# Optimization experiments

Hardware: AMD Instinct MI355X
Metric: run time of the kernel (lower is better)

Reference implementation:

```python
import jax, jax.numpy as jnp
import numpy as np

B, A, M = 64, 128, 8          # batch (conformers), atoms, ensemble models
D, O0, O2, O4, O6 = 384, 256, 192, 160, 1  # AEV dim and padded layer out dims


def setup_inputs() -> dict:
    key = jax.random.key(0)
    ks = jax.random.split(key, 10)
    return {
        "species": jax.random.randint(ks[0], (B, A), 0, 4),
        "aev": jax.random.normal(ks[1], (B, A, D), dtype=jnp.float32),
        "w0": jax.random.normal(ks[2], (1, A, M, O0, D), dtype=jnp.float32),
        "b0": jax.random.normal(ks[3], (1, A, M, O0, 1), dtype=jnp.float32),
        "w2": jax.random.normal(ks[4], (1, A, M, O2, O0), dtype=jnp.float32),
        "b2": jax.random.normal(ks[5], (1, A, M, O2, 1), dtype=jnp.float32),
        "w4": jax.random.normal(ks[6], (1, A, M, O4, O2), dtype=jnp.float32),
        "b4": jax.random.normal(ks[7], (1, A, M, O4, 1), dtype=jnp.float32),
        "w6": jax.random.normal(ks[8], (1, A, M, O6, O4), dtype=jnp.float32),
        "b6": jax.random.normal(ks[9], (1, A, M, O6, 1), dtype=jnp.float32),
    }


def _celu(x, alpha=0.1):
    # F.celu(x, alpha) = max(0,x) + min(0, alpha*(exp(x/alpha)-1))
    return jnp.where(x > 0, x, alpha * jnp.expm1(x / alpha))


def reference(species, aev, w0, b0, w2, b2, w4, b4, w6, b6):
    # batchedLinear(v, W, b) == W @ v + b per (atom, model) block,
    # broadcast over batch; first layer broadcasts the model dim (1 -> M).
    # x: [B, A, M, out]
    x = jnp.einsum('zamoi,bai->bamo', w0, aev) + b0[..., 0]
    x = _celu(x)
    x = jnp.einsum('zamoi,bami->bamo', w2, x) + b2[..., 0]
    x = _celu(x)
    x = jnp.einsum('zamoi,bami->bamo', w4, x) + b4[..., 0]
    x = _celu(x)
    x = jnp.einsum('zamoi,bami->bamo', w6, x) + b6[..., 0]
    # sum over atoms, models, out (and the trailing singleton), divide by n_models
    energies = jnp.sum(x, axis=(1, 2, 3)) / M  # [B]
    return species, energies
```

## Files before the change

### kernel.cpp

```cpp
#include <hip/hip_runtime.h>

#define B_ 64
#define A_ 128
#define M_ 8
#define D_ 384
#define O0_ 256
#define O2_ 192
#define O4_ 160

typedef float f32x4 __attribute__((ext_vector_type(4)));
typedef _Float16 f16x8 __attribute__((ext_vector_type(8)));
typedef _Float16 f16x4 __attribute__((ext_vector_type(4)));

__device__ __forceinline__ float celu_f(float x) {
    return x > 0.f ? x : 0.1f * (__expf(x * 10.f) - 1.f);
}

__device__ __forceinline__ f32x4 zero4() {
    f32x4 v; v[0] = 0.f; v[1] = 0.f; v[2] = 0.f; v[3] = 0.f; return v;
}

template<int K, int O, int OPITCH, bool SWZ_OUT>
__device__ __forceinline__ void layer_mfma(const float* __restrict__ W,
                                           const float* __restrict__ bias,
                                           const _Float16* Xin, _Float16* Xout,
                                           int wave, int col, int quad)
{
    constexpr int KSTEPS = K / 32;
    constexpr int OTILES = O / 16;
    for (int ot = wave; ot < OTILES; ot += 4) {
        const float* wrow = W + (size_t)(ot * 16 + col) * K + quad * 8;
        f32x4 acc[4];
        #pragma unroll
        for (int nt = 0; nt < 4; ++nt) acc[nt] = zero4();
        #pragma unroll
        for (int ks = 0; ks < KSTEPS; ++ks) {
            f32x4 wlo = *(const f32x4*)(wrow + ks * 32);
            f32x4 whi = *(const f32x4*)(wrow + ks * 32 + 4);
            f16x8 afr;
            afr[0] = (_Float16)wlo[0]; afr[1] = (_Float16)wlo[1];
            afr[2] = (_Float16)wlo[2]; afr[3] = (_Float16)wlo[3];
            afr[4] = (_Float16)whi[0]; afr[5] = (_Float16)whi[1];
            afr[6] = (_Float16)whi[2]; afr[7] = (_Float16)whi[3];
            #pragma unroll
            for (int nt = 0; nt < 4; ++nt) {
                const int b = nt * 16 + col;
                const int c = ks * 4 + quad;
                const f16x8 bfr = *(const f16x8*)(Xin + b * K + ((c ^ (b & 7)) * 8));
                acc[nt] = __builtin_amdgcn_mfma_f32_16x16x32_f16(afr, bfr, acc[nt], 0, 0, 0);
            }
        }
        const f32x4 bias4 = *(const f32x4*)(bias + ot * 16 + quad * 4);
        const int o0 = ot * 16 + quad * 4;
        #pragma unroll
        for (int nt = 0; nt < 4; ++nt) {
            const int b = nt * 16 + col;
            f16x4 h;
            #pragma unroll
            for (int r = 0; r < 4; ++r) h[r] = (_Float16)celu_f(acc[nt][r] + bias4[r]);
            if (SWZ_OUT) {
                const int c = o0 >> 3;
                *(f16x4*)(Xout + b * OPITCH + ((c ^ (b & 7)) * 8) + (o0 & 7)) = h;
            } else {
                *(f16x4*)(Xout + b * OPITCH + o0) = h;
            }
        }
    }
}

__global__ __launch_bounds__(256, 2) void nn_kernel(
    const float* __restrict__ aev,
    const float* __restrict__ w0, const float* __restrict__ b0,
    const float* __restrict__ w2, const float* __restrict__ b2,
    const float* __restrict__ w4, const float* __restrict__ b4,
    const float* __restrict__ w6, const float* __restrict__ b6,
    float* __restrict__ out)
{
    __shared__ __align__(16) unsigned char smem_raw[57344];
    _Float16* const lds = (_Float16*)smem_raw;

    const int tid  = threadIdx.x;
    const int wave = tid >> 6;
    const int lane = tid & 63;
    const int col  = lane & 15;
    const int quad = lane >> 4;

    const int a  = blockIdx.x >> 3;
    const int m  = blockIdx.x & 7;
    const int am = a * 8 + m;

    const float* w0p = w0 + (size_t)am * O0_ * D_;
    const float* b0p = b0 + am * O0_;
    const float* w2p = w2 + (size_t)am * O2_ * O0_;
    const float* b2p = b2 + am * O2_;
    const float* w4p = w4 + (size_t)am * O4_ * O2_;
    const float* b4p = b4 + am * O4_;
    const float* w6p = w6 + am * O4_;
    const float  b6v = b6[am];

    _Float16* bufStage = lds;
    _Float16* X0 = lds + 12288;
    _Float16* X2 = lds;
    _Float16* X4 = lds + 12288;
    float* part = (float*)(smem_raw + 45568);

    f32x4 acc0[4][4];
    #pragma unroll
    for (int i = 0; i < 4; ++i)
        #pragma unroll
        for (int nt = 0; nt < 4; ++nt) acc0[i][nt] = zero4();

    #pragma unroll
    for (int kc = 0; kc < 2; ++kc) {
        if (kc) __syncthreads();
        #pragma unroll
        for (int it = 0; it < 6; ++it) {
            const int idx = tid + it * 256;
            const int b = idx / 24;
            const int c = idx % 24;
            const float* src = aev + ((size_t)b * A_ + a) * D_ + kc * 192 + c * 8;
            f32x4 lo = *(const f32x4*)src;
            f32x4 hi = *(const f32x4*)(src + 4);
            f16x8 h;
            h[0] = (_Float16)lo[0]; h[1] = (_Float16)lo[1];
            h[2] = (_Float16)lo[2]; h[3] = (_Float16)lo[3];
            h[4] = (_Float16)hi[0]; h[5] = (_Float16)hi[1];
            h[6] = (_Float16)hi[2]; h[7] = (_Float16)hi[3];
            *(f16x8*)(bufStage + b * 192 + ((c ^ (b & 7)) * 8)) = h;
        }
        __syncthreads();
        #pragma unroll
        for (int i = 0; i < 4; ++i) {
            const int ot = wave + i * 4;
            const float* wrow = w0p + (size_t)(ot * 16 + col) * D_ + kc * 192 + quad * 8;
            #pragma unroll
            for (int ks = 0; ks < 6; ++ks) {
                f32x4 wlo = *(const f32x4*)(wrow + ks * 32);
                f32x4 whi = *(const f32x4*)(wrow + ks * 32 + 4);
                f16x8 afr;
                afr[0] = (_Float16)wlo[0]; afr[1] = (_Float16)wlo[1];
                afr[2] = (_Float16)wlo[2]; afr[3] = (_Float16)wlo[3];
                afr[4] = (_Float16)whi[0]; afr[5] = (_Float16)whi[1];
                afr[6] = (_Float16)whi[2]; afr[7] = (_Float16)whi[3];
                #pragma unroll
                for (int nt = 0; nt < 4; ++nt) {
                    const int b = nt * 16 + col;
                    const int c = ks * 4 + quad;
                    const f16x8 bfr = *(const f16x8*)(bufStage + b * 192 + ((c ^ (b & 7)) * 8));
                    acc0[i][nt] = __builtin_amdgcn_mfma_f32_16x16x32_f16(afr, bfr, acc0[i][nt], 0, 0, 0);
                }
            }
        }
    }
    #pragma unroll
    for (int i = 0; i < 4; ++i) {
        const int ot = wave + i * 4;
        const f32x4 bias4 = *(const f32x4*)(b0p + ot * 16 + quad * 4);
        const int o0 = ot * 16 + quad * 4;
        #pragma unroll
        for (int nt = 0; nt < 4; ++nt) {
            const int b = nt * 16 + col;
            f16x4 h;
            #pragma unroll
            for (int r = 0; r < 4; ++r) h[r] = (_Float16)celu_f(acc0[i][nt][r] + bias4[r]);
            const int c = o0 >> 3;
            *(f16x4*)(X0 + b * 256 + ((c ^ (b & 7)) * 8) + (o0 & 7)) = h;
        }
    }
    __syncthreads();

    layer_mfma<256, 192, 192, true>(w2p, b2p, X0, X2, wave, col, quad);
    __syncthreads();

    layer_mfma<192, 160, 164, false>(w4p, b4p, X2, X4, wave, col, quad);
    __syncthreads();

    {
        const int b  = tid & 63;
        const int pt = tid >> 6;
        const _Float16* xrow = X4 + b * 164 + pt * 40;
        const float* wseg = w6p + pt * 40;
        float s = 0.f;
        #pragma unroll
        for (int j = 0; j < 10; ++j) {
            f32x4 wv = *(const f32x4*)(wseg + j * 4);
            f16x4 xv = *(const f16x4*)(xrow + j * 4);
            s += wv[0] * (float)xv[0] + wv[1] * (float)xv[1] +
                 wv[2] * (float)xv[2] + wv[3] * (float)xv[3];
        }
        part[tid] = s;
    }
    __syncthreads();
    if (tid < 64) {
        const float x6 = part[tid] + part[tid + 64] + part[tid + 128] + part[tid + 192] + b6v;
        atomicAdd(out + B_ * A_ + tid, x6 * 0.125f);
    }
}

__global__ void init_out_kernel(const int* __restrict__ species, float* __restrict__ out) {
    const int i = blockIdx.x * 256 + threadIdx.x;
    if (i < B_ * A_) out[i] = (float)species[i];
    if (i < B_) out[B_ * A_ + i] = 0.f;
}

extern "C" void kernel_launch(void* const* d_in, const int* in_sizes, int n_in,
                              void* d_out, int out_size, void* d_ws, size_t ws_size,
                              hipStream_t stream) {
    const int*   species = (const int*)d_in[0];
    const float* aev = (const float*)d_in[1];
    const float* w0  = (const float*)d_in[2];
    const float* b0  = (const float*)d_in[3];
    const float* w2  = (const float*)d_in[4];
    const float* b2  = (const float*)d_in[5];
    const float* w4  = (const float*)d_in[6];
    const float* b4  = (const float*)d_in[7];
    const float* w6  = (const float*)d_in[8];
    const float* b6  = (const float*)d_in[9];
    float* out = (float*)d_out;

    hipLaunchKernelGGL(init_out_kernel, dim3(32), dim3(256), 0, stream, species, out);
    hipLaunchKernelGGL(nn_kernel, dim3(A_ * M_), dim3(256), 0, stream,
                       aev, w0, b0, w2, b2, w4, b4, w6, b6, out);
}
```

Measured before the change: 745.8 us.

## Shrink LDS footprint to fit three blocks per CU

Stages the AEV input in three 128-wide chunks instead of two 192-wide chunks. Layer-2 outputs are held in registers so X2 can overwrite X0's space after a barrier, letting the shared-memory allocation drop to about 49 KB. Launch bounds are raised to three blocks per CU so more blocks can be resident to hide the global weight-load latency. In exchange it adds barriers, extra aev staging passes, and register pressure under a tighter per-thread register budget, which could cause spills.

```diff
diff --git a/kernel.cpp b/kernel.cpp
--- a/kernel.cpp
+++ b/kernel.cpp
@@ -20,11 +20,22 @@
     f32x4 v; v[0] = 0.f; v[1] = 0.f; v[2] = 0.f; v[3] = 0.f; return v;
 }
 
-template<int K, int O, int OPITCH, bool SWZ_OUT>
-__device__ __forceinline__ void layer_mfma(const float* __restrict__ W,
-                                           const float* __restrict__ bias,
-                                           const _Float16* Xin, _Float16* Xout,
-                                           int wave, int col, int quad)
+__device__ __forceinline__ f16x8 cvt_w8(const float* p) {
+    f32x4 lo = *(const f32x4*)p;
+    f32x4 hi = *(const f32x4*)(p + 4);
+    f16x8 h;
+    h[0] = (_Float16)lo[0]; h[1] = (_Float16)lo[1];
+    h[2] = (_Float16)lo[2]; h[3] = (_Float16)lo[3];
+    h[4] = (_Float16)hi[0]; h[5] = (_Float16)hi[1];
+    h[6] = (_Float16)hi[2]; h[7] = (_Float16)hi[3];
+    return h;
+}
+
+template<int K, int O, int OPITCH>
+__device__ __forceinline__ void layer_mfma_plain(const float* __restrict__ W,
+                                                 const float* __restrict__ bias,
+                                                 const _Float16* Xin, _Float16* Xout,
+                                                 int wave, int col, int quad)
 {
     constexpr int KSTEPS = K / 32;
     constexpr int OTILES = O / 16;
@@ -35,13 +46,7 @@
         for (int nt = 0; nt < 4; ++nt) acc[nt] = zero4();
         #pragma unroll
         for (int ks = 0; ks < KSTEPS; ++ks) {
-            f32x4 wlo = *(const f32x4*)(wrow + ks * 32);
-            f32x4 whi = *(const f32x4*)(wrow + ks * 32 + 4);
-            f16x8 afr;
-            afr[0] = (_Float16)wlo[0]; afr[1] = (_Float16)wlo[1];
-            afr[2] = (_Float16)wlo[2]; afr[3] = (_Float16)wlo[3];
-            afr[4] = (_Float16)whi[0]; afr[5] = (_Float16)whi[1];
-            afr[6] = (_Float16)whi[2]; afr[7] = (_Float16)whi[3];
+            const f16x8 afr = cvt_w8(wrow + ks * 32);
             #pragma unroll
             for (int nt = 0; nt < 4; ++nt) {
                 const int b = nt * 16 + col;
@@ -58,17 +63,12 @@
             f16x4 h;
             #pragma unroll
             for (int r = 0; r < 4; ++r) h[r] = (_Float16)celu_f(acc[nt][r] + bias4[r]);
-            if (SWZ_OUT) {
-                const int c = o0 >> 3;
-                *(f16x4*)(Xout + b * OPITCH + ((c ^ (b & 7)) * 8) + (o0 & 7)) = h;
-            } else {
-                *(f16x4*)(Xout + b * OPITCH + o0) = h;
-            }
-        }
-    }
-}
-
-__global__ __launch_bounds__(256, 2) void nn_kernel(
+            *(f16x4*)(Xout + b * OPITCH + o0) = h;
+        }
+    }
+}
+
+__global__ __launch_bounds__(256, 3) void nn_kernel(
     const float* __restrict__ aev,
     const float* __restrict__ w0, const float* __restrict__ b0,
     const float* __restrict__ w2, const float* __restrict__ b2,
@@ -76,7 +76,7 @@
     const float* __restrict__ w6, const float* __restrict__ b6,
     float* __restrict__ out)
 {
-    __shared__ __align__(16) unsigned char smem_raw[57344];
+    __shared__ __align__(16) unsigned char smem_raw[50176];
     _Float16* const lds = (_Float16*)smem_raw;
 
     const int tid  = threadIdx.x;
@@ -99,10 +99,10 @@
     const float  b6v = b6[am];
 
     _Float16* bufStage = lds;
-    _Float16* X0 = lds + 12288;
+    _Float16* X0 = lds + 8192;
     _Float16* X2 = lds;
     _Float16* X4 = lds + 12288;
-    float* part = (float*)(smem_raw + 45568);
+    float* part = (float*)(smem_raw + 49152);
 
     f32x4 acc0[4][4];
     #pragma unroll
@@ -111,42 +111,29 @@
         for (int nt = 0; nt < 4; ++nt) acc0[i][nt] = zero4();
 
     #pragma unroll
-    for (int kc = 0; kc < 2; ++kc) {
+    for (int kc = 0; kc < 3; ++kc) {
         if (kc) __syncthreads();
         #pragma unroll
-        for (int it = 0; it < 6; ++it) {
+        for (int it = 0; it < 4; ++it) {
             const int idx = tid + it * 256;
-            const int b = idx / 24;
-            const int c = idx % 24;
-            const float* src = aev + ((size_t)b * A_ + a) * D_ + kc * 192 + c * 8;
-            f32x4 lo = *(const f32x4*)src;
-            f32x4 hi = *(const f32x4*)(src + 4);
-            f16x8 h;
-            h[0] = (_Float16)lo[0]; h[1] = (_Float16)lo[1];
-            h[2] = (_Float16)lo[2]; h[3] = (_Float16)lo[3];
-            h[4] = (_Float16)hi[0]; h[5] = (_Float16)hi[1];
-            h[6] = (_Float16)hi[2]; h[7] = (_Float16)hi[3];
-            *(f16x8*)(bufStage + b * 192 + ((c ^ (b & 7)) * 8)) = h;
+            const int b = idx >> 4;
+            const int c = idx & 15;
+            const float* src = aev + ((size_t)b * A_ + a) * D_ + kc * 128 + c * 8;
+            *(f16x8*)(bufStage + b * 128 + ((c ^ (b & 7)) * 8)) = cvt_w8(src);
         }
         __syncthreads();
         #pragma unroll
         for (int i = 0; i < 4; ++i) {
             const int ot = wave + i * 4;
-            const float* wrow = w0p + (size_t)(ot * 16 + col) * D_ + kc * 192 + quad * 8;
-            #pragma unroll
-            for (int ks = 0; ks < 6; ++ks) {
-                f32x4 wlo = *(const f32x4*)(wrow + ks * 32);
-                f32x4 whi = *(const f32x4*)(wrow + ks * 32 + 4);
-                f16x8 afr;
-                afr[0] = (_Float16)wlo[0]; afr[1] = (_Float16)wlo[1];
-                afr[2] = (_Float16)wlo[2]; afr[3] = (_Float16)wlo[3];
-                afr[4] = (_Float16)whi[0]; afr[5] = (_Float16)whi[1];
-                afr[6] = (_Float16)whi[2]; afr[7] = (_Float16)whi[3];
+            const float* wrow = w0p + (size_t)(ot * 16 + col) * D_ + kc * 128 + quad * 8;
+            #pragma unroll
+            for (int ks = 0; ks < 4; ++ks) {
+                const f16x8 afr = cvt_w8(wrow + ks * 32);
                 #pragma unroll
                 for (int nt = 0; nt < 4; ++nt) {
                     const int b = nt * 16 + col;
                     const int c = ks * 4 + quad;
-                    const f16x8 bfr = *(const f16x8*)(bufStage + b * 192 + ((c ^ (b & 7)) * 8));
+                    const f16x8 bfr = *(const f16x8*)(bufStage + b * 128 + ((c ^ (b & 7)) * 8));
                     acc0[i][nt] = __builtin_amdgcn_mfma_f32_16x16x32_f16(afr, bfr, acc0[i][nt], 0, 0, 0);
                 }
             }
@@ -169,10 +156,46 @@
     }
     __syncthreads();
 
-    layer_mfma<256, 192, 192, true>(w2p, b2p, X0, X2, wave, col, quad);
-    __syncthreads();
-
-    layer_mfma<192, 160, 164, false>(w4p, b4p, X2, X4, wave, col, quad);
+    f16x4 h2[3][4];
+    #pragma unroll
+    for (int i = 0; i < 3; ++i) {
+        const int ot = wave + i * 4;
+        const float* wrow = w2p + (size_t)(ot * 16 + col) * O0_ + quad * 8;
+        f32x4 acc[4];
+        #pragma unroll
+        for (int nt = 0; nt < 4; ++nt) acc[nt] = zero4();
+        #pragma unroll
+        for (int ks = 0; ks < 8; ++ks) {
+            const f16x8 afr = cvt_w8(wrow + ks * 32);
+            #pragma unroll
+            for (int nt = 0; nt < 4; ++nt) {
+                const int b = nt * 16 + col;
+                const int c = ks * 4 + quad;
+                const f16x8 bfr = *(const f16x8*)(X0 + b * 256 + ((c ^ (b & 7)) * 8));
+                acc[nt] = __builtin_amdgcn_mfma_f32_16x16x32_f16(afr, bfr, acc[nt], 0, 0, 0);
+            }
+        }
+        const f32x4 bias4 = *(const f32x4*)(b2p + ot * 16 + quad * 4);
+        #pragma unroll
+        for (int nt = 0; nt < 4; ++nt) {
+            #pragma unroll
+            for (int r = 0; r < 4; ++r) h2[i][nt][r] = (_Float16)celu_f(acc[nt][r] + bias4[r]);
+        }
+    }
+    __syncthreads();
+    #pragma unroll
+    for (int i = 0; i < 3; ++i) {
+        const int o0 = (wave + i * 4) * 16 + quad * 4;
+        const int c = o0 >> 3;
+        #pragma unroll
+        for (int nt = 0; nt < 4; ++nt) {
+            const int b = nt * 16 + col;
+            *(f16x4*)(X2 + b * 192 + ((c ^ (b & 7)) * 8) + (o0 & 7)) = h2[i][nt];
+        }
+    }
+    __syncthreads();
+
+    layer_mfma_plain<192, 160, 164>(w4p, b4p, X2, X4, wave, col, quad);
     __syncthreads();
 
     {
```

Result: slower. 783.5 us (+5.1%).
